# Performance work log

Measured on AMD Instinct MI355X. Metric: run time of the kernel, lower is better.

## Reference

```python
import jax, jax.numpy as jnp
import numpy as np
from jax import lax

TAU = 2.0
EPS = 1e-5
STEP = 10      # time steps
RATIO = 4     # TIM_ratio
HEADS = 16
SCALE = 0.25


@jax.custom_vjp
def _spike(v):
    return (v > 0.0).astype(v.dtype)

def _spike_fwd(v):
    return _spike(v), v

def _spike_bwd(v, g):
    alpha = 4.0  # sigmoid surrogate gradient
    s = jax.nn.sigmoid(alpha * v)
    return (g * alpha * s * (1.0 - s),)

_spike.defvjp(_spike_fwd, _spike_bwd)


def lif(x, vth=1.0):
    """LIF neuron over leading time dim: mem += (x-mem)/tau, fire, hard reset (detached)."""
    def step(mem, xt):
        mem = mem + (xt - mem) / TAU
        s = _spike(mem - vth)
        mem = mem * (1.0 - lax.stop_gradient(s))
        return mem, s
    _, out = lax.scan(step, jnp.zeros_like(x[0]), x)
    return out


def bn(x, p, axis):
    """Inference-mode batchnorm; p = stacked (gamma, beta, mean, var) along dim 0."""
    g, b, m, v = p
    sh = [1] * x.ndim
    sh[axis] = -1
    return (x - m.reshape(sh)) / jnp.sqrt(v.reshape(sh) + EPS) * g.reshape(sh) + b.reshape(sh)


def conv3d(x, w, groups=1):
    return lax.conv_general_dilated(
        x, w, window_strides=(1, 1, 1), padding=[(1, 1)] * 3,
        dimension_numbers=('NCDHW', 'OIDHW', 'NCDHW'),
        feature_group_count=groups)


def tim(x, up_w, bn1, down_w, bn2):
    # x: (T, B, C, H, W); conv3d treats T as channels, (C,H,W) as the volume
    T, B, C, H, W = x.shape
    y = conv3d(jnp.swapaxes(x, 0, 1), up_w)                      # (B, T*R, C, H, W)
    y = jnp.swapaxes(bn(y, bn1, 1), 0, 1)                        # (T*R, B, C, H, W)
    # MyNode reshapes (T*R*B, ...) into STEP time chunks of size R*B
    y = lif(y.reshape(STEP, -1, C, H, W)).reshape(T * RATIO, B, C, H, W)
    y = conv3d(jnp.swapaxes(y, 0, 1), down_w, groups=STEP)       # (B, T, C, H, W)
    y = jnp.swapaxes(bn(y, bn2, 1), 0, 1)                        # (T, B, C, H, W)
    return lif(y)


def ssa(x, q_w, q_bn, k_w, k_bn, v_w, v_bn, proj_w, proj_bn,
        tim_up_w, tim_bn1, tim_down_w, tim_bn2):
    T, B, C, H, W = x.shape
    N = H * W
    d = C // HEADS
    xf = x.reshape(T * B, C, N)

    def branch(w, bnp):
        y = bn(jnp.einsum('oc,bcn->bon', w, xf), bnp, 1).reshape(T, B, C, H, W)
        y = tim(y, tim_up_w, tim_bn1, tim_down_w, tim_bn2)       # binary spikes
        y = y.reshape(T, B, C, N).transpose(0, 1, 3, 2)          # (T, B, N, C)
        return y.reshape(T, B, N, HEADS, d).transpose(0, 1, 3, 2, 4)  # (T, B, h, N, d)

    q = branch(q_w, q_bn)
    k = branch(k_w, k_bn)
    v = branch(v_w, v_bn)
    attn = jnp.einsum('tbhnd,tbhmd->tbhnm', q, k)                # no softmax (spiking attn)
    o = jnp.einsum('tbhnm,tbhmd->tbhnd', attn, v) * SCALE
    o = o.transpose(0, 1, 2, 4, 3).reshape(T, B, C, N)           # merge (h, d) -> C
    o = lif(o, vth=0.5)                                          # attn_lif, threshold 0.5
    o = bn(jnp.einsum('oc,tbcn->tbon', proj_w, o), proj_bn, 2)   # 1x1 conv1d + BN1d
    return lif(o).reshape(T, B, C, H, W)


def mlp(x, fc1_w, fc1_b, fc1_bn, fc2_w, fc2_b, fc2_bn):
    T, B, C, H, W = x.shape
    y = jnp.einsum('oc,tbchw->tbohw', fc1_w, x) + fc1_b.reshape(1, 1, -1, 1, 1)
    y = lif(bn(y, fc1_bn, 2))
    y = jnp.einsum('oc,tbchw->tbohw', fc2_w, y) + fc2_b.reshape(1, 1, -1, 1, 1)
    return lif(bn(y, fc2_bn, 2))


def setup_inputs() -> dict:
    key = jax.random.key(0)
    ks = jax.random.split(key, 24)
    T, B, C, H, W = 10, 4, 256, 16, 16
    HID = 1024

    def bnp(k, c):
        k1, k2, k3, k4 = jax.random.split(k, 4)
        gamma = jax.random.uniform(k1, (c,), minval=0.5, maxval=1.5)
        beta = 0.1 * jax.random.normal(k2, (c,))
        mean = 0.1 * jax.random.normal(k3, (c,))
        var = jax.random.uniform(k4, (c,), minval=0.5, maxval=1.5)
        return jnp.stack([gamma, beta, mean, var]).astype(jnp.float32)

    inp = {
        'x': jax.random.normal(ks[0], (T, B, C, H, W), jnp.float32),
        'q_w': jax.random.normal(ks[1], (C, C)) / np.sqrt(C),
        'q_bn': bnp(ks[2], C),
        'k_w': jax.random.normal(ks[3], (C, C)) / np.sqrt(C),
        'k_bn': bnp(ks[4], C),
        'v_w': jax.random.normal(ks[5], (C, C)) / np.sqrt(C),
        'v_bn': bnp(ks[6], C),
        'proj_w': jax.random.normal(ks[7], (C, C)) / np.sqrt(C),
        'proj_bn': bnp(ks[8], C),
        'tim_up_w': jax.random.normal(ks[9], (STEP * RATIO, STEP, 3, 3, 3)) / np.sqrt(STEP * 27),
        'tim_bn1': bnp(ks[10], STEP * RATIO),
        'tim_down_w': jax.random.normal(ks[11], (STEP, RATIO, 3, 3, 3)) / np.sqrt(RATIO * 27),
        'tim_bn2': bnp(ks[12], STEP),
        'fc1_w': jax.random.normal(ks[13], (HID, C)) / np.sqrt(C),
        'fc1_b': 0.1 * jax.random.normal(ks[14], (HID,)),
        'fc1_bn': bnp(ks[15], HID),
        'fc2_w': jax.random.normal(ks[16], (C, HID)) / np.sqrt(HID),
        'fc2_b': 0.1 * jax.random.normal(ks[17], (C,)),
        'fc2_bn': bnp(ks[18], C),
    }
    return {k: v.astype(jnp.float32) for k, v in inp.items()}


def reference(x, q_w, q_bn, k_w, k_bn, v_w, v_bn, proj_w, proj_bn,
              tim_up_w, tim_bn1, tim_down_w, tim_bn2,
              fc1_w, fc1_b, fc1_bn, fc2_w, fc2_b, fc2_bn):
    h = x + ssa(x, q_w, q_bn, k_w, k_bn, v_w, v_bn, proj_w, proj_bn,
                tim_up_w, tim_bn1, tim_down_w, tim_bn2)
    return h + mlp(h, fc1_w, fc1_b, fc1_bn, fc2_w, fc2_b, fc2_bn)
```

## Files before the change

kernel.cpp:

```cpp
#include <hip/hip_runtime.h>
#include <cstdint>
#include <cstddef>

#define EPSF 1e-5f

typedef __attribute__((ext_vector_type(8))) short short8;
typedef __attribute__((ext_vector_type(4))) float f32x4;

__device__ __forceinline__ unsigned short bf16_rne(float f) {
    unsigned int u = __float_as_uint(f);
    u += 0x7FFFu + ((u >> 16) & 1u);
    return (unsigned short)(u >> 16);
}
__device__ __forceinline__ float bf16f(unsigned short h) {
    return __uint_as_float(((unsigned int)h) << 16);
}

__device__ __forceinline__ void split_pack_body(
    const float* __restrict__ W, unsigned short* __restrict__ P,
    int O, int K, int idx)
{
    const int OT = O >> 4, KT = K >> 5;
    const int lane = idx & 63, tile = idx >> 6;
    const int kt = tile % KT, ot = tile / KT;
    const int quad = lane >> 4, l15 = lane & 15;
    const int row = ot * 16 + l15, col = kt * 32 + quad * 8;
    const size_t base = ((size_t)ot * KT + kt) * 512 + lane * 8;
    const size_t sOff = (size_t)OT * KT * 512;
#pragma unroll
    for (int j = 0; j < 8; ++j) {
        float v = W[(size_t)row * K + col + j];
        unsigned short h1 = bf16_rne(v);
        float r = v - bf16f(h1);
        unsigned short h2 = bf16_rne(r);
        float r2 = r - bf16f(h2);
        P[base + j] = h1;
        P[sOff + base + j] = h2;
        P[2 * sOff + base + j] = bf16_rne(r2);
    }
}

__global__ __launch_bounds__(256) void split_pack_k(
    const float* __restrict__ W, unsigned short* __restrict__ P, int O, int K)
{
    int idx = blockIdx.x * 256 + threadIdx.x;
    if (idx >= (O * K) >> 3) return;
    split_pack_body(W, P, O, K, idx);
}

struct SplitArgs { const float* W[3]; unsigned short* P[3]; };
__global__ __launch_bounds__(256) void split_pack3_k(SplitArgs sa, int O, int K)
{
    int idx = blockIdx.x * 256 + threadIdx.x;
    if (idx >= (O * K) >> 3) return;
    split_pack_body(sa.W[blockIdx.y], sa.P[blockIdx.y], O, K, idx);
}

__global__ __launch_bounds__(256) void bpack_k(
    const float* __restrict__ B, unsigned short* __restrict__ BP,
    int K, int N, int S)
{
    const int KT = K >> 5, NT16 = N >> 4;
    int idx = blockIdx.x * 256 + threadIdx.x;
    if (idx >= S * NT16 * KT * 64) return;
    const int lane = idx & 63;
    int tile = idx >> 6;
    const int kt = tile % KT; tile /= KT;
    const int n16 = tile % NT16; const int s = tile / NT16;
    const int quad = lane >> 4, l15 = lane & 15;
    const size_t base = (size_t)idx * 8;
    const size_t sOff = (size_t)S * NT16 * KT * 512;
    const float* src = B + (size_t)s * K * N + (size_t)(kt * 32 + quad * 8) * N
                         + n16 * 16 + l15;
#pragma unroll
    for (int j = 0; j < 8; ++j) {
        float v = src[(size_t)j * N];
        unsigned short h1 = bf16_rne(v);
        float r = v - bf16f(h1);
        unsigned short h2 = bf16_rne(r);
        float r2 = r - bf16f(h2);
        BP[base + j] = h1;
        BP[sOff + base + j] = h2;
        BP[2 * sOff + base + j] = bf16_rne(r2);
    }
}

struct MArgs { const unsigned short* W[3]; float* Out[3]; const float* bn[3]; };

#define MM(AP, BQ)                                                            \
    {                                                                         \
        _Pragma("unroll") for (int mt = 0; mt < 2; ++mt)                      \
        _Pragma("unroll") for (int nt = 0; nt < 2; ++nt)                      \
            acc[mt][nt] = __builtin_amdgcn_mfma_f32_16x16x32_bf16(            \
                Af[AP][mt], Bf[BQ][nt], acc[mt][nt], 0, 0, 0);                \
    }

__global__ __launch_bounds__(256, 4) void mfma_gemm3(
    MArgs a, const unsigned short* __restrict__ BP,
    const float* __restrict__ bias, int O, int K, int N)
{
    const unsigned short* __restrict__ W = a.W[blockIdx.z];
    float* __restrict__ Out = a.Out[blockIdx.z];
    const float* __restrict__ bnp = a.bn[blockIdx.z];
    const int OT = O >> 4, KT = K >> 5, NT16 = N >> 4;
    const size_t sA = (size_t)OT * KT * 512;
    const size_t sB = (size_t)gridDim.y * NT16 * KT * 512;

    const int slice  = blockIdx.y;
    const int tilesn = N >> 6;
    const int to = (blockIdx.x / tilesn) << 6;
    const int tn = (blockIdx.x % tilesn) << 6;
    const int tid = threadIdx.x;
    const int wid = tid >> 6, lane = tid & 63;
    const int quad = lane >> 4, l15 = lane & 15;
    const int wm = (wid >> 1) << 5, wn = (wid & 1) << 5;
    const int oti0 = (to + wm) >> 4;
    const int n160 = (tn + wn) >> 4;

    f32x4 acc[2][2];
#pragma unroll
    for (int mt = 0; mt < 2; ++mt)
#pragma unroll
        for (int nt = 0; nt < 2; ++nt)
#pragma unroll
            for (int r = 0; r < 4; ++r) acc[mt][nt][r] = 0.0f;

    for (int kt = 0; kt < KT; ++kt) {
        short8 Af[3][2], Bf[3][2];
#pragma unroll
        for (int mt = 0; mt < 2; ++mt) {
            const size_t fa = ((size_t)(oti0 + mt) * KT + kt) * 512 + lane * 8;
            Af[0][mt] = *(const short8*)(W + fa);
            Af[1][mt] = *(const short8*)(W + sA + fa);
            Af[2][mt] = *(const short8*)(W + 2 * sA + fa);
        }
#pragma unroll
        for (int nt = 0; nt < 2; ++nt) {
            const size_t fb =
                (((size_t)slice * NT16 + n160 + nt) * KT + kt) * 512 + lane * 8;
            Bf[0][nt] = *(const short8*)(BP + fb);
            Bf[1][nt] = *(const short8*)(BP + sB + fb);
            Bf[2][nt] = *(const short8*)(BP + 2 * sB + fb);
        }
        MM(0, 0) MM(0, 1) MM(1, 0) MM(0, 2) MM(1, 1) MM(2, 0)
    }

    float* Op = Out + (size_t)slice * O * N;
#pragma unroll
    for (int mt = 0; mt < 2; ++mt) {
#pragma unroll
        for (int r = 0; r < 4; ++r) {
            const int o = to + wm + (mt << 4) + (quad << 2) + r;
            float g = bnp[o], bb = bnp[O + o], m = bnp[2 * O + o], vv = bnp[3 * O + o];
            float sq = sqrtf(vv + EPSF);
            float bs = bias ? bias[o] : 0.0f;
#pragma unroll
            for (int nt = 0; nt < 2; ++nt) {
                const int n = tn + wn + (nt << 4) + l15;
                float val = acc[mt][nt][r] + bs;
                Op[(size_t)o * N + n] = (val - m) / sq * g + bb;
            }
        }
    }
}

__global__ __launch_bounds__(256, 2) void mfma_gemm2(
    MArgs a, const float* __restrict__ X, const float* __restrict__ bias,
    int O, int K, int N)
{
    const unsigned short* __restrict__ W = a.W[blockIdx.z];
    float* __restrict__ Out = a.Out[blockIdx.z];
    const float* __restrict__ bnp = a.bn[blockIdx.z];
    const int OT = O >> 4, KT = K >> 5;
    const size_t sOff = (size_t)OT * KT * 512;

    __shared__ float Bsm[2][32][65];

    const int slice  = blockIdx.y;
    const int tilesn = N >> 6;
    const int to = (blockIdx.x / tilesn) << 6;
    const int tn = (blockIdx.x % tilesn) << 6;
    const int tid = threadIdx.x;
    const int wid = tid >> 6, lane = tid & 63;
    const int quad = lane >> 4, l15 = lane & 15;
    const int wm = (wid >> 1) << 5, wn = (wid & 1) << 5;
    const int oti0 = (to + wm) >> 4;

    f32x4 acc[2][2];
#pragma unroll
    for (int mt = 0; mt < 2; ++mt)
#pragma unroll
        for (int nt = 0; nt < 2; ++nt)
#pragma unroll
            for (int r = 0; r < 4; ++r) acc[mt][nt][r] = 0.0f;

    const float* Xs = X + (size_t)slice * K * N;
    const int nn = tid & 63, r0 = tid >> 6;

    float breg[8];
#pragma unroll
    for (int it = 0; it < 8; ++it)
        breg[it] = Xs[(size_t)(it * 4 + r0) * N + tn + nn];
#pragma unroll
    for (int it = 0; it < 8; ++it)
        Bsm[0][it * 4 + r0][nn] = breg[it];
    __syncthreads();

    for (int kt = 0; kt < KT; ++kt) {
        const int cur = kt & 1;
        if (kt + 1 < KT) {
#pragma unroll
            for (int it = 0; it < 8; ++it)
                breg[it] = Xs[(size_t)((kt + 1) * 32 + it * 4 + r0) * N + tn + nn];
        }
        short8 Af[3][2];
#pragma unroll
        for (int mt = 0; mt < 2; ++mt) {
            const size_t fb = ((size_t)(oti0 + mt) * KT + kt) * 512 + lane * 8;
            Af[0][mt] = *(const short8*)(W + fb);
            Af[1][mt] = *(const short8*)(W + sOff + fb);
            Af[2][mt] = *(const short8*)(W + 2 * sOff + fb);
        }
        short8 Bf[1][2];
#pragma unroll
        for (int nt = 0; nt < 2; ++nt) {
            const int bc = wn + (nt << 4) + l15;
#pragma unroll
            for (int j = 0; j < 8; ++j)
                Bf[0][nt][j] = (short)bf16_rne(Bsm[cur][(quad << 3) + j][bc]);
        }
        MM(0, 0) MM(1, 0) MM(2, 0)
        if (kt + 1 < KT) {
            const int nxt = cur ^ 1;
#pragma unroll
            for (int it = 0; it < 8; ++it)
                Bsm[nxt][it * 4 + r0][nn] = breg[it];
        }
        __syncthreads();
    }

    float* Op = Out + (size_t)slice * O * N;
#pragma unroll
    for (int mt = 0; mt < 2; ++mt) {
#pragma unroll
        for (int r = 0; r < 4; ++r) {
            const int o = to + wm + (mt << 4) + (quad << 2) + r;
            float g = bnp[o], bb = bnp[O + o], m = bnp[2 * O + o], vv = bnp[3 * O + o];
            float sq = sqrtf(vv + EPSF);
            float bs = bias ? bias[o] : 0.0f;
#pragma unroll
            for (int nt = 0; nt < 2; ++nt) {
                const int n = tn + wn + (nt << 4) + l15;
                float val = acc[mt][nt][r] + bs;
                Op[(size_t)o * N + n] = (val - m) / sq * g + bb;
            }
        }
    }
}

__global__ __launch_bounds__(256) void wt_k(
    const float* __restrict__ up_w, float* __restrict__ WT)
{
    int idx = blockIdx.x * 256 + threadIdx.x;
    if (idx >= 12960) return;
    int slot = idx % 48, tq = idx / 48;
    int g = slot / 12, u = slot % 12;
    float v = 0.0f;
    if (u < 10) v = up_w[(4 * u + g) * 270 + tq];
    WT[idx] = v;
}

__global__ __launch_bounds__(256, 6) void tim_up4(
    const float* __restrict__ Y, const float* __restrict__ WT,
    const float* __restrict__ bn1, float* __restrict__ SPK)
{
    __shared__ float smem[5 * 3 * 200];
    const int c = blockIdx.x;
    const int b = blockIdx.y >> 1, half = blockIdx.y & 1;
    const int tid = threadIdx.x;
    const int lane = tid & 63;
    const int g = __builtin_amdgcn_readfirstlane(tid >> 6);
    const int hb2 = (lane >> 4) << 1;
    const int wc = lane & 15;

    float acc[2][10];
#pragma unroll
    for (int i = 0; i < 2; ++i)
#pragma unroll
        for (int u = 0; u < 10; ++u) acc[i][u] = 0.0f;

#pragma unroll 1
    for (int ph = 0; ph < 2; ++ph) {
        __syncthreads();
        for (int idx = tid; idx < 3000; idx += 256) {
            int t = ph * 5 + idx / 600, rem = idx % 600;
            int cc = rem / 200, p = rem % 200;
            int rr = p / 20, col = p % 20;
            int h = half * 8 + rr - 1, ww = col - 1;
            int cs = c + cc - 1;
            float v = 0.0f;
            if (cs >= 0 && cs < 256 && h >= 0 && h < 16 && ww >= 0 && ww < 16)
                v = Y[((t * 4 + b) * 256 + cs) * 256 + h * 16 + ww];
            smem[idx] = v;
        }
        __syncthreads();

#pragma unroll 1
        for (int tt = 0; tt < 5; ++tt) {
            const int t = ph * 5 + tt;
#pragma unroll
            for (int kd = 0; kd < 3; ++kd) {
                const float* sp = &smem[tt * 600 + kd * 200 + hb2 * 20 + wc];
                float vr[4][3];
#pragma unroll
                for (int r = 0; r < 4; ++r)
#pragma unroll
                    for (int kc = 0; kc < 3; ++kc)
                        vr[r][kc] = sp[r * 20 + kc];
#pragma unroll
                for (int q = 0; q < 9; ++q) {
                    const int kh = q / 3, kw = q % 3;
                    const float4* wp =
                        (const float4*)&WT[(t * 27 + kd * 9 + q) * 48 + g * 12];
                    float4 w0 = wp[0], w1 = wp[1];
                    float4 w2 = wp[2];
                    float wr[10] = {w0.x, w0.y, w0.z, w0.w, w1.x,
                                    w1.y, w1.z, w1.w, w2.x, w2.y};
#pragma unroll
                    for (int u = 0; u < 10; ++u)
#pragma unroll
                        for (int i = 0; i < 2; ++i)
                            acc[i][u] = fmaf(wr[u], vr[i + kh][kw], acc[i][u]);
                }
            }
        }
    }

#pragma unroll
    for (int i = 0; i < 2; ++i) {
        const int h = half * 8 + hb2 + i;
        float mem = 0.0f;
#pragma unroll
        for (int s = 0; s < 10; ++s) {
            const int uc = 4 * s + g;
            float ga = bn1[uc], be = bn1[40 + uc], mu = bn1[80 + uc], va = bn1[120 + uc];
            float xv = (acc[i][s] - mu) / sqrtf(va + EPSF) * ga + be;
            mem += (xv - mem) * 0.5f;
            float spk = mem > 1.0f ? 1.0f : 0.0f;
            SPK[(((size_t)b * 40 + uc) * 256 + c) * 256 + h * 16 + wc] = spk;
            mem = spk > 0.0f ? 0.0f : mem;
        }
    }
}

__global__ __launch_bounds__(256) void tim_down_pre(
    const float* __restrict__ SPK, const float* __restrict__ w,
    const float* __restrict__ bn2, float* __restrict__ PreY)
{
    __shared__ float smem[4 * 3 * 324];
    const int c = blockIdx.x, b = blockIdx.y, t = blockIdx.z;
    const int tid = threadIdx.x;
    for (int idx = tid; idx < 3888; idx += 256) {
        int r = idx / 972, rem = idx % 972;
        int cc = rem / 324, p = rem % 324;
        int hh = p / 18 - 1, ww = p % 18 - 1;
        int cs = c + cc - 1;
        float v = 0.0f;
        if (cs >= 0 && cs < 256 && hh >= 0 && hh < 16 && ww >= 0 && ww < 16)
            v = SPK[(((size_t)b * 40 + 4 * t + r) * 256 + cs) * 256 + hh * 16 + ww];
        smem[idx] = v;
    }
    __syncthreads();
    const int h = tid >> 4, wq = tid & 15;
    float a = 0.0f;
#pragma unroll
    for (int r = 0; r < 4; ++r)
#pragma unroll
        for (int kd = 0; kd < 3; ++kd) {
            const float* wp = w + ((t * 4 + r) * 3 + kd) * 9;
#pragma unroll
            for (int kh = 0; kh < 3; ++kh)
#pragma unroll
                for (int kw = 0; kw < 3; ++kw)
                    a = fmaf(wp[kh * 3 + kw],
                             smem[r * 972 + kd * 324 + (h + kh) * 18 + (wq + kw)], a);
        }
    a = (a - bn2[20 + t]) / sqrtf(bn2[30 + t] + EPSF) * bn2[t] + bn2[10 + t];
    PreY[((t * 4 + b) * 256 + c) * 256 + tid] = a;
}

__global__ __launch_bounds__(256) void lif_down(
    const float* __restrict__ PreY, float* __restrict__ S)
{
    const int idx = blockIdx.x * 256 + threadIdx.x;
    float mem = 0.0f;
    for (int t = 0; t < 10; ++t) {
        float v = PreY[t * 262144 + idx];
        mem += (v - mem) * 0.5f;
        float spk = mem > 1.0f ? 1.0f : 0.0f;
        S[t * 262144 + idx] = spk;
        mem = spk > 0.0f ? 0.0f : mem;
    }
}

__global__ __launch_bounds__(256) void ktv_k(
    const float* __restrict__ SK, const float* __restrict__ SV,
    float* __restrict__ KTV)
{
    __shared__ float ks[16 * 257], vs[16 * 257];
    const int bi = blockIdx.x;
    const int t = bi >> 6, b = (bi >> 4) & 3, hd = bi & 15;
    const int tid = threadIdx.x;
    for (int i = tid; i < 4096; i += 256) {
        int row = i >> 8, col = i & 255;
        ks[row * 257 + col] = SK[((t * 4 + b) * 256 + hd * 16 + row) * 256 + col];
        vs[row * 257 + col] = SV[((t * 4 + b) * 256 + hd * 16 + row) * 256 + col];
    }
    __syncthreads();
    const int j = tid >> 4, j2 = tid & 15;
    float a0 = 0.0f, a1 = 0.0f, a2 = 0.0f, a3 = 0.0f;
#pragma unroll 4
    for (int n = 0; n < 256; n += 4) {
        a0 = fmaf(ks[j * 257 + n + 0], vs[j2 * 257 + n + 0], a0);
        a1 = fmaf(ks[j * 257 + n + 1], vs[j2 * 257 + n + 1], a1);
        a2 = fmaf(ks[j * 257 + n + 2], vs[j2 * 257 + n + 2], a2);
        a3 = fmaf(ks[j * 257 + n + 3], vs[j2 * 257 + n + 3], a3);
    }
    KTV[((t * 4 + b) * 16 + hd) * 256 + tid] = (a0 + a1) + (a2 + a3);
}

__global__ __launch_bounds__(256) void attn_k(
    const float* __restrict__ SQ, const float* __restrict__ KTV,
    float* __restrict__ OSPK)
{
    __shared__ float kt[2560];
    __shared__ float qs[16 * 17];
    const int x = blockIdx.x;
    const int b = x >> 8, hd = (x >> 4) & 15, ng = x & 15;
    const int tid = threadIdx.x;
    const int j2 = tid >> 4, nl = tid & 15;
    const int n = ng * 16 + nl;
    for (int i = tid; i < 2560; i += 256) {
        int t = i >> 8;
        kt[i] = KTV[((t * 4 + b) * 16 + hd) * 256 + (i & 255)];
    }
    float mem = 0.0f;
    for (int t = 0; t < 10; ++t) {
        __syncthreads();
        qs[nl * 17 + j2] = SQ[((t * 4 + b) * 256 + hd * 16 + j2) * 256 + n];
        __syncthreads();
        float a = 0.0f;
#pragma unroll
        for (int j = 0; j < 16; ++j)
            a = fmaf(qs[nl * 17 + j], kt[t * 256 + j * 16 + j2], a);
        a *= 0.25f;
        mem += (a - mem) * 0.5f;
        float spk = mem > 0.5f ? 1.0f : 0.0f;
        OSPK[((t * 4 + b) * 256 + hd * 16 + j2) * 256 + n] = spk;
        mem = spk > 0.0f ? 0.0f : mem;
    }
}

__global__ __launch_bounds__(256) void ssa_lif_res(
    const float* __restrict__ P, const float* __restrict__ x,
    float* __restrict__ H)
{
    const int idx = blockIdx.x * 256 + threadIdx.x;
    float mem = 0.0f;
    for (int t = 0; t < 10; ++t) {
        float v = P[t * 262144 + idx];
        mem += (v - mem) * 0.5f;
        float spk = mem > 1.0f ? 1.0f : 0.0f;
        H[t * 262144 + idx] = x[t * 262144 + idx] + spk;
        mem = spk > 0.0f ? 0.0f : mem;
    }
}

__global__ __launch_bounds__(256) void lif_ip(float* __restrict__ A)
{
    const int idx = blockIdx.x * 256 + threadIdx.x;
    float mem = 0.0f;
    for (int t = 0; t < 10; ++t) {
        float v = A[t * 1048576 + idx];
        mem += (v - mem) * 0.5f;
        float spk = mem > 1.0f ? 1.0f : 0.0f;
        A[t * 1048576 + idx] = spk;
        mem = spk > 0.0f ? 0.0f : mem;
    }
}

__global__ __launch_bounds__(256) void final_k(
    const float* __restrict__ P, const float* __restrict__ H,
    float* __restrict__ out)
{
    const int idx = blockIdx.x * 256 + threadIdx.x;
    float mem = 0.0f;
    for (int t = 0; t < 10; ++t) {
        float v = P[t * 262144 + idx];
        mem += (v - mem) * 0.5f;
        float spk = mem > 1.0f ? 1.0f : 0.0f;
        out[t * 262144 + idx] = H[t * 262144 + idx] + spk;
        mem = spk > 0.0f ? 0.0f : mem;
    }
}

extern "C" void kernel_launch(void* const* d_in, const int* in_sizes, int n_in,
                              void* d_out, int out_size, void* d_ws, size_t ws_size,
                              hipStream_t stream)
{
    const float* x        = (const float*)d_in[0];
    const float* q_w      = (const float*)d_in[1];
    const float* q_bn     = (const float*)d_in[2];
    const float* k_w      = (const float*)d_in[3];
    const float* k_bn     = (const float*)d_in[4];
    const float* v_w      = (const float*)d_in[5];
    const float* v_bn     = (const float*)d_in[6];
    const float* proj_w   = (const float*)d_in[7];
    const float* proj_bn  = (const float*)d_in[8];
    const float* up_w     = (const float*)d_in[9];
    const float* bn1      = (const float*)d_in[10];
    const float* down_w   = (const float*)d_in[11];
    const float* bn2      = (const float*)d_in[12];
    const float* fc1_w    = (const float*)d_in[13];
    const float* fc1_b    = (const float*)d_in[14];
    const float* fc1_bn   = (const float*)d_in[15];
    const float* fc2_w    = (const float*)d_in[16];
    const float* fc2_b    = (const float*)d_in[17];
    const float* fc2_bn   = (const float*)d_in[18];

    float* ws   = (float*)d_ws;
    float* Y    = ws;
    float* ASPK = Y + 2621440;
    float* SQ   = ASPK + 10485760;
    float* SK   = SQ + 2621440;
    float* SV   = SK + 2621440;
    float* KTV  = SV + 2621440;
    float* WT   = KTV;

    float* Yb[3] = {Y, SK, SV};
    float* Sb[3] = {SQ, SK, SV};

    unsigned short* qs_s = (unsigned short*)ASPK;
    unsigned short* ks_s = qs_s + 196608;
    unsigned short* vs_s = qs_s + 393216;
    unsigned short* xp_s = qs_s + 589824;

    wt_k<<<51, 256, 0, stream>>>(up_w, WT);
    SplitArgs sa;
    sa.W[0] = q_w; sa.W[1] = k_w; sa.W[2] = v_w;
    sa.P[0] = qs_s; sa.P[1] = ks_s; sa.P[2] = vs_s;
    split_pack3_k<<<dim3(32, 3), 256, 0, stream>>>(sa, 256, 256);
    bpack_k<<<1280, 256, 0, stream>>>(x, xp_s, 256, 256, 40);

    MArgs qkv;
    qkv.W[0] = qs_s;  qkv.W[1] = ks_s;  qkv.W[2] = vs_s;
    qkv.Out[0] = Yb[0]; qkv.Out[1] = Yb[1]; qkv.Out[2] = Yb[2];
    qkv.bn[0] = q_bn; qkv.bn[1] = k_bn; qkv.bn[2] = v_bn;
    mfma_gemm3<<<dim3(16, 40, 3), 256, 0, stream>>>(qkv, xp_s, nullptr, 256, 256, 256);

    for (int br = 0; br < 3; ++br) {
        tim_up4<<<dim3(256, 8), 256, 0, stream>>>(Yb[br], WT, bn1, ASPK);
        tim_down_pre<<<dim3(256, 4, 10), 256, 0, stream>>>(ASPK, down_w, bn2, Y);
        lif_down<<<1024, 256, 0, stream>>>(Y, Sb[br]);
    }

    ktv_k<<<640, 256, 0, stream>>>(SK, SV, KTV);
    attn_k<<<1024, 256, 0, stream>>>(SQ, KTV, Y);

    unsigned short* pj_s = (unsigned short*)ASPK;
    split_pack_k<<<32, 256, 0, stream>>>(proj_w, pj_s, 256, 256);
    MArgs gp; gp.W[0] = gp.W[1] = gp.W[2] = pj_s;
    gp.Out[0] = gp.Out[1] = gp.Out[2] = SQ;
    gp.bn[0] = gp.bn[1] = gp.bn[2] = proj_bn;
    mfma_gemm2<<<dim3(16, 40, 1), 256, 0, stream>>>(gp, Y, nullptr, 256, 256, 256);
    ssa_lif_res<<<1024, 256, 0, stream>>>(SQ, x, SV);

    unsigned short* f1b = (unsigned short*)SQ;
    bpack_k<<<1280, 256, 0, stream>>>(SV, f1b, 256, 256, 40);
    unsigned short* f1_s = (unsigned short*)Y;
    split_pack_k<<<128, 256, 0, stream>>>(fc1_w, f1_s, 1024, 256);
    MArgs g1; g1.W[0] = g1.W[1] = g1.W[2] = f1_s;
    g1.Out[0] = g1.Out[1] = g1.Out[2] = ASPK;
    g1.bn[0] = g1.bn[1] = g1.bn[2] = fc1_bn;
    mfma_gemm3<<<dim3(64, 40, 1), 256, 0, stream>>>(g1, f1b, fc1_b, 1024, 256, 256);
    lif_ip<<<4096, 256, 0, stream>>>(ASPK);

    unsigned short* f2_s = (unsigned short*)Y;
    split_pack_k<<<128, 256, 0, stream>>>(fc2_w, f2_s, 256, 1024);
    MArgs g2; g2.W[0] = g2.W[1] = g2.W[2] = f2_s;
    g2.Out[0] = g2.Out[1] = g2.Out[2] = SK;
    g2.bn[0] = g2.bn[1] = g2.bn[2] = fc2_bn;
    mfma_gemm2<<<dim3(16, 40, 1), 256, 0, stream>>>(g2, ASPK, fc2_b, 256, 1024, 256);
    final_k<<<1024, 256, 0, stream>>>(SK, SV, (float*)d_out);
}
```

Before: 749.9 us.

## Batch TIM branches, store spikes as bytes, pack spikes directly for MFMA GEMMs

The three TIM branches now run as single launches over a z-dimension instead of a host loop of three kernel triples. The intermediate spike tensor is stored as uint8 rather than float32, which cuts its write and read traffic. The attention and fc1 LIF kernels now write binary spikes straight into the bf16 MFMA-packed B layout, so proj and fc2 use mfma_gemm3 with a single B split and drop the fp32-to-bf16 conversion in shared memory. The trade-off is scattered packed writes and larger fused grids.

```diff
diff --git a/kernel.cpp b/kernel.cpp
--- a/kernel.cpp
+++ b/kernel.cpp
@@ -97,7 +97,7 @@
 
 __global__ __launch_bounds__(256, 4) void mfma_gemm3(
     MArgs a, const unsigned short* __restrict__ BP,
-    const float* __restrict__ bias, int O, int K, int N)
+    const float* __restrict__ bias, int O, int K, int N, int nB)
 {
     const unsigned short* __restrict__ W = a.W[blockIdx.z];
     float* __restrict__ Out = a.Out[blockIdx.z];
@@ -139,104 +139,16 @@
             const size_t fb =
                 (((size_t)slice * NT16 + n160 + nt) * KT + kt) * 512 + lane * 8;
             Bf[0][nt] = *(const short8*)(BP + fb);
-            Bf[1][nt] = *(const short8*)(BP + sB + fb);
-            Bf[2][nt] = *(const short8*)(BP + 2 * sB + fb);
-        }
-        MM(0, 0) MM(0, 1) MM(1, 0) MM(0, 2) MM(1, 1) MM(2, 0)
-    }
-
-    float* Op = Out + (size_t)slice * O * N;
-#pragma unroll
-    for (int mt = 0; mt < 2; ++mt) {
-#pragma unroll
-        for (int r = 0; r < 4; ++r) {
-            const int o = to + wm + (mt << 4) + (quad << 2) + r;
-            float g = bnp[o], bb = bnp[O + o], m = bnp[2 * O + o], vv = bnp[3 * O + o];
-            float sq = sqrtf(vv + EPSF);
-            float bs = bias ? bias[o] : 0.0f;
-#pragma unroll
-            for (int nt = 0; nt < 2; ++nt) {
-                const int n = tn + wn + (nt << 4) + l15;
-                float val = acc[mt][nt][r] + bs;
-                Op[(size_t)o * N + n] = (val - m) / sq * g + bb;
+            if (nB == 3) {
+                Bf[1][nt] = *(const short8*)(BP + sB + fb);
+                Bf[2][nt] = *(const short8*)(BP + 2 * sB + fb);
             }
         }
-    }
-}
-
-__global__ __launch_bounds__(256, 2) void mfma_gemm2(
-    MArgs a, const float* __restrict__ X, const float* __restrict__ bias,
-    int O, int K, int N)
-{
-    const unsigned short* __restrict__ W = a.W[blockIdx.z];
-    float* __restrict__ Out = a.Out[blockIdx.z];
-    const float* __restrict__ bnp = a.bn[blockIdx.z];
-    const int OT = O >> 4, KT = K >> 5;
-    const size_t sOff = (size_t)OT * KT * 512;
-
-    __shared__ float Bsm[2][32][65];
-
-    const int slice  = blockIdx.y;
-    const int tilesn = N >> 6;
-    const int to = (blockIdx.x / tilesn) << 6;
-    const int tn = (blockIdx.x % tilesn) << 6;
-    const int tid = threadIdx.x;
-    const int wid = tid >> 6, lane = tid & 63;
-    const int quad = lane >> 4, l15 = lane & 15;
-    const int wm = (wid >> 1) << 5, wn = (wid & 1) << 5;
-    const int oti0 = (to + wm) >> 4;
-
-    f32x4 acc[2][2];
-#pragma unroll
-    for (int mt = 0; mt < 2; ++mt)
-#pragma unroll
-        for (int nt = 0; nt < 2; ++nt)
-#pragma unroll
-            for (int r = 0; r < 4; ++r) acc[mt][nt][r] = 0.0f;
-
-    const float* Xs = X + (size_t)slice * K * N;
-    const int nn = tid & 63, r0 = tid >> 6;
-
-    float breg[8];
-#pragma unroll
-    for (int it = 0; it < 8; ++it)
-        breg[it] = Xs[(size_t)(it * 4 + r0) * N + tn + nn];
-#pragma unroll
-    for (int it = 0; it < 8; ++it)
-        Bsm[0][it * 4 + r0][nn] = breg[it];
-    __syncthreads();
-
-    for (int kt = 0; kt < KT; ++kt) {
-        const int cur = kt & 1;
-        if (kt + 1 < KT) {
-#pragma unroll
-            for (int it = 0; it < 8; ++it)
-                breg[it] = Xs[(size_t)((kt + 1) * 32 + it * 4 + r0) * N + tn + nn];
-        }
-        short8 Af[3][2];
-#pragma unroll
-        for (int mt = 0; mt < 2; ++mt) {
-            const size_t fb = ((size_t)(oti0 + mt) * KT + kt) * 512 + lane * 8;
-            Af[0][mt] = *(const short8*)(W + fb);
-            Af[1][mt] = *(const short8*)(W + sOff + fb);
-            Af[2][mt] = *(const short8*)(W + 2 * sOff + fb);
-        }
-        short8 Bf[1][2];
-#pragma unroll
-        for (int nt = 0; nt < 2; ++nt) {
-            const int bc = wn + (nt << 4) + l15;
-#pragma unroll
-            for (int j = 0; j < 8; ++j)
-                Bf[0][nt][j] = (short)bf16_rne(Bsm[cur][(quad << 3) + j][bc]);
-        }
-        MM(0, 0) MM(1, 0) MM(2, 0)
-        if (kt + 1 < KT) {
-            const int nxt = cur ^ 1;
-#pragma unroll
-            for (int it = 0; it < 8; ++it)
-                Bsm[nxt][it * 4 + r0][nn] = breg[it];
-        }
-        __syncthreads();
+        if (nB == 3) {
+            MM(0, 0) MM(0, 1) MM(1, 0) MM(0, 2) MM(1, 1) MM(2, 0)
+        } else {
+            MM(0, 0) MM(1, 0) MM(2, 0)
+        }
     }
 
     float* Op = Out + (size_t)slice * O * N;
@@ -270,11 +182,15 @@
     WT[idx] = v;
 }
 
-__global__ __launch_bounds__(256, 6) void tim_up4(
-    const float* __restrict__ Y, const float* __restrict__ WT,
-    const float* __restrict__ bn1, float* __restrict__ SPK)
+struct TimArgs { const float* Y[3]; };
+
+__global__ __launch_bounds__(256, 8) void tim_up5(
+    TimArgs ta, const float* __restrict__ WT,
+    const float* __restrict__ bn1, unsigned char* __restrict__ USPK)
 {
     __shared__ float smem[5 * 3 * 200];
+    const float* __restrict__ Y = ta.Y[blockIdx.z];
+    unsigned char* __restrict__ SPK = USPK + (size_t)blockIdx.z * 10485760;
     const int c = blockIdx.x;
     const int b = blockIdx.y >> 1, half = blockIdx.y & 1;
     const int tid = threadIdx.x;
@@ -346,19 +262,25 @@
             float ga = bn1[uc], be = bn1[40 + uc], mu = bn1[80 + uc], va = bn1[120 + uc];
             float xv = (acc[i][s] - mu) / sqrtf(va + EPSF) * ga + be;
             mem += (xv - mem) * 0.5f;
-            float spk = mem > 1.0f ? 1.0f : 0.0f;
+            unsigned char spk = mem > 1.0f ? 1 : 0;
             SPK[(((size_t)b * 40 + uc) * 256 + c) * 256 + h * 16 + wc] = spk;
-            mem = spk > 0.0f ? 0.0f : mem;
-        }
-    }
-}
-
-__global__ __launch_bounds__(256) void tim_down_pre(
-    const float* __restrict__ SPK, const float* __restrict__ w,
-    const float* __restrict__ bn2, float* __restrict__ PreY)
+            mem = spk ? 0.0f : mem;
+        }
+    }
+}
+
+struct PtrArgs { float* p[3]; };
+struct CPtrArgs { const float* p[3]; };
+
+__global__ __launch_bounds__(256) void tim_down_pre5(
+    const unsigned char* __restrict__ USPK, const float* __restrict__ w,
+    const float* __restrict__ bn2, PtrArgs PY)
 {
     __shared__ float smem[4 * 3 * 324];
-    const int c = blockIdx.x, b = blockIdx.y, t = blockIdx.z;
+    const int br = blockIdx.z / 10, t = blockIdx.z % 10;
+    const unsigned char* __restrict__ SPK = USPK + (size_t)br * 10485760;
+    float* __restrict__ PreY = PY.p[br];
+    const int c = blockIdx.x, b = blockIdx.y;
     const int tid = threadIdx.x;
     for (int idx = tid; idx < 3888; idx += 256) {
         int r = idx / 972, rem = idx % 972;
@@ -367,7 +289,7 @@
         int cs = c + cc - 1;
         float v = 0.0f;
         if (cs >= 0 && cs < 256 && hh >= 0 && hh < 16 && ww >= 0 && ww < 16)
-            v = SPK[(((size_t)b * 40 + 4 * t + r) * 256 + cs) * 256 + hh * 16 + ww];
+            v = (float)SPK[(((size_t)b * 40 + 4 * t + r) * 256 + cs) * 256 + hh * 16 + ww];
         smem[idx] = v;
     }
     __syncthreads();
@@ -389,9 +311,10 @@
     PreY[((t * 4 + b) * 256 + c) * 256 + tid] = a;
 }
 
-__global__ __launch_bounds__(256) void lif_down(
-    const float* __restrict__ PreY, float* __restrict__ S)
-{
+__global__ __launch_bounds__(256) void lif_down3(CPtrArgs PY, PtrArgs SB)
+{
+    const float* __restrict__ PreY = PY.p[blockIdx.y];
+    float* __restrict__ S = SB.p[blockIdx.y];
     const int idx = blockIdx.x * 256 + threadIdx.x;
     float mem = 0.0f;
     for (int t = 0; t < 10; ++t) {
@@ -429,9 +352,9 @@
     KTV[((t * 4 + b) * 16 + hd) * 256 + tid] = (a0 + a1) + (a2 + a3);
 }
 
-__global__ __launch_bounds__(256) void attn_k(
+__global__ __launch_bounds__(256) void attn_k2(
     const float* __restrict__ SQ, const float* __restrict__ KTV,
-    float* __restrict__ OSPK)
+    unsigned short* __restrict__ PSPK)
 {
     __shared__ float kt[2560];
     __shared__ float qs[16 * 17];
@@ -444,6 +367,9 @@
         int t = i >> 8;
         kt[i] = KTV[((t * 4 + b) * 16 + hd) * 256 + (i & 255)];
     }
+    const int c = hd * 16 + j2;
+    const int ktile = c >> 5, quad = (c >> 3) & 3, jj = c & 7;
+    const int lane = quad * 16 + nl;
     float mem = 0.0f;
     for (int t = 0; t < 10; ++t) {
         __syncthreads();
@@ -456,7 +382,8 @@
         a *= 0.25f;
         mem += (a - mem) * 0.5f;
         float spk = mem > 0.5f ? 1.0f : 0.0f;
-        OSPK[((t * 4 + b) * 256 + hd * 16 + j2) * 256 + n] = spk;
+        PSPK[((((size_t)(t * 4 + b) * 16 + ng) * 8 + ktile) * 512) + lane * 8 + jj] =
+            spk > 0.0f ? (unsigned short)0x3F80 : (unsigned short)0;
         mem = spk > 0.0f ? 0.0f : mem;
     }
 }
@@ -476,15 +403,22 @@
     }
 }
 
-__global__ __launch_bounds__(256) void lif_ip(float* __restrict__ A)
+__global__ __launch_bounds__(256) void lif_pack(
+    const float* __restrict__ A, unsigned short* __restrict__ PB)
 {
     const int idx = blockIdx.x * 256 + threadIdx.x;
+    const int b = idx >> 18, rem = idx & 262143;
+    const int hid = rem >> 8, hw = rem & 255;
+    const int ktile = hid >> 5, quad = (hid >> 3) & 3, jj = hid & 7;
+    const int n16 = hw >> 4, l15 = hw & 15;
+    const int lane = quad * 16 + l15;
     float mem = 0.0f;
     for (int t = 0; t < 10; ++t) {
         float v = A[t * 1048576 + idx];
         mem += (v - mem) * 0.5f;
         float spk = mem > 1.0f ? 1.0f : 0.0f;
-        A[t * 1048576 + idx] = spk;
+        PB[((((size_t)(t * 4 + b) * 16 + n16) * 32 + ktile) * 512) + lane * 8 + jj] =
+            spk > 0.0f ? (unsigned short)0x3F80 : (unsigned short)0;
         mem = spk > 0.0f ? 0.0f : mem;
     }
 }
@@ -537,9 +471,6 @@
     float* KTV  = SV + 2621440;
     float* WT   = KTV;
 
-    float* Yb[3] = {Y, SK, SV};
-    float* Sb[3] = {SQ, SK, SV};
-
     unsigned short* qs_s = (unsigned short*)ASPK;
     unsigned short* ks_s = qs_s + 196608;
     unsigned short* vs_s = qs_s + 393216;
@@ -554,25 +485,31 @@
 
     MArgs qkv;
     qkv.W[0] = qs_s;  qkv.W[1] = ks_s;  qkv.W[2] = vs_s;
-    qkv.Out[0] = Yb[0]; qkv.Out[1] = Yb[1]; qkv.Out[2] = Yb[2];
+    qkv.Out[0] = Y; qkv.Out[1] = SK; qkv.Out[2] = SV;
     qkv.bn[0] = q_bn; qkv.bn[1] = k_bn; qkv.bn[2] = v_bn;
-    mfma_gemm3<<<dim3(16, 40, 3), 256, 0, stream>>>(qkv, xp_s, nullptr, 256, 256, 256);
-
-    for (int br = 0; br < 3; ++br) {
-        tim_up4<<<dim3(256, 8), 256, 0, stream>>>(Yb[br], WT, bn1, ASPK);
-        tim_down_pre<<<dim3(256, 4, 10), 256, 0, stream>>>(ASPK, down_w, bn2, Y);
-        lif_down<<<1024, 256, 0, stream>>>(Y, Sb[br]);
-    }
+    mfma_gemm3<<<dim3(16, 40, 3), 256, 0, stream>>>(qkv, xp_s, nullptr, 256, 256, 256, 3);
+
+    unsigned char* USPK = (unsigned char*)ASPK;
+    TimArgs ta; ta.Y[0] = Y; ta.Y[1] = SK; ta.Y[2] = SV;
+    tim_up5<<<dim3(256, 8, 3), 256, 0, stream>>>(ta, WT, bn1, USPK);
+
+    PtrArgs PY; PY.p[0] = Y; PY.p[1] = SK; PY.p[2] = SV;
+    tim_down_pre5<<<dim3(256, 4, 30), 256, 0, stream>>>(USPK, down_w, bn2, PY);
+
+    CPtrArgs PYc; PYc.p[0] = Y; PYc.p[1] = SK; PYc.p[2] = SV;
+    PtrArgs SB; SB.p[0] = SQ; SB.p[1] = SK; SB.p[2] = SV;
+    lif_down3<<<dim3(1024, 3), 256, 0, stream>>>(PYc, SB);
 
     ktv_k<<<640, 256, 0, stream>>>(SK, SV, KTV);
-    attn_k<<<1024, 256, 0, stream>>>(SQ, KTV, Y);
+    unsigned short* PSPK = (unsigned short*)Y;
+    attn_k2<<<1024, 256, 0, stream>>>(SQ, KTV, PSPK);
 
     unsigned short* pj_s = (unsigned short*)ASPK;
     split_pack_k<<<32, 256, 0, stream>>>(proj_w, pj_s, 256, 256);
     MArgs gp; gp.W[0] = gp.W[1] = gp.W[2] = pj_s;
     gp.Out[0] = gp.Out[1] = gp.Out[2] = SQ;
     gp.bn[0] = gp.bn[1] = gp.bn[2] = proj_bn;
-    mfma_gemm2<<<dim3(16, 40, 1), 256, 0, stream>>>(gp, Y, nullptr, 256, 256, 256);
+    mfma_gemm3<<<dim3(16, 40, 1), 256, 0, stream>>>(gp, PSPK, nullptr, 256, 256, 256, 1);
     ssa_lif_res<<<1024, 256, 0, stream>>>(SQ, x, SV);
 
     unsigned short* f1b = (unsigned short*)SQ;
@@ -582,14 +519,15 @@
     MArgs g1; g1.W[0] = g1.W[1] = g1.W[2] = f1_s;
     g1.Out[0] = g1.Out[1] = g1.Out[2] = ASPK;
     g1.bn[0] = g1.bn[1] = g1.bn[2] = fc1_bn;
-    mfma_gemm3<<<dim3(64, 40, 1), 256, 0, stream>>>(g1, f1b, fc1_b, 1024, 256, 256);
-    lif_ip<<<4096, 256, 0, stream>>>(ASPK);
-
+    mfma_gemm3<<<dim3(64, 40, 1), 256, 0, stream>>>(g1, f1b, fc1_b, 1024, 256, 256, 3);
+
+    unsigned short* PB2 = (unsigned short*)SQ;
+    lif_pack<<<4096, 256, 0, stream>>>(ASPK, PB2);
     unsigned short* f2_s = (unsigned short*)Y;
     split_pack_k<<<128, 256, 0, stream>>>(fc2_w, f2_s, 256, 1024);
     MArgs g2; g2.W[0] = g2.W[1] = g2.W[2] = f2_s;
-    g2.Out[0] = g2.Out[1] = g2.Out[2] = SK;
+    g2.Out[0] = g2.Out[1] = g2.Out[2] = ASPK;
     g2.bn[0] = g2.bn[1] = g2.bn[2] = fc2_bn;
-    mfma_gemm2<<<dim3(16, 40, 1), 256, 0, stream>>>(g2, ASPK, fc2_b, 256, 1024, 256);
-    final_k<<<1024, 256, 0, stream>>>(SK, SV, (float*)d_out);
-}
+    mfma_gemm3<<<dim3(16, 40, 1), 256, 0, stream>>>(g2, PB2, fc2_b, 256, 1024, 256, 1);
+    final_k<<<1024, 256, 0, stream>>>(ASPK, SV, (float*)d_out);
+}
```

Result: faster. 682.5 us (-9.0%).
